# Kernel optimization log

Hardware: AMD Instinct MI355X
Metric: run time of the kernel (lower is better)

The kernel has to match this reference:

```python
import jax, jax.numpy as jnp
import numpy as np

D, N, F_IN, F_OUT = 2, 4096, 128, 128
DENSITY = 0.005  # avg degree ~20 per row in the 0/1 attention graphs
NEG_INF = -1e30


def setup_inputs() -> dict:
    key = jax.random.key(0)
    ks = jax.random.split(key, 12)
    X = jax.random.normal(ks[0], (D, N, F_IN), dtype=jnp.float32)
    # Dense Laplacian operator used in torch.sparse.mm(L[i], h_p); scaled so tanh stays non-degenerate
    L = jax.random.normal(ks[1], (D, N, N), dtype=jnp.float32) / np.float32(np.sqrt(N))
    # Upper/lower adjacency: 0/1 matrices (GATLayer extracts edges via adj == 1)
    L_u = (jax.random.uniform(ks[2], (D, N, N)) < DENSITY).astype(jnp.float32)
    L_d = (jax.random.uniform(ks[3], (D, N, N)) < DENSITY).astype(jnp.float32)
    s = np.float32(0.05)
    Wp = jax.random.normal(ks[4], (D, F_IN, F_OUT), dtype=jnp.float32) * s
    Ws = jax.random.normal(ks[5], (D, F_IN, F_OUT), dtype=jnp.float32) * s
    Wu = jax.random.normal(ks[6], (D, F_IN, F_OUT), dtype=jnp.float32) * s
    au1 = jax.random.normal(ks[7], (D, F_OUT), dtype=jnp.float32) * s
    au2 = jax.random.normal(ks[8], (D, F_OUT), dtype=jnp.float32) * s
    Wd = jax.random.normal(ks[9], (D, F_IN, F_OUT), dtype=jnp.float32) * s
    ad1 = jax.random.normal(ks[10], (D, F_OUT), dtype=jnp.float32) * s
    ad2 = jax.random.normal(ks[11], (D, F_OUT), dtype=jnp.float32) * s
    return {"X": X, "L": L, "L_u": L_u, "L_d": L_d,
            "Wp": Wp, "Ws": Ws, "Wu": Wu, "au1": au1, "au2": au2,
            "Wd": Wd, "ad1": ad1, "ad2": ad2, "dimensions": D}


def _gat(x, adj, W, a1, a2):
    # GATLayer.forward with boundary=False: linear -> edge scores -> LeakyReLU ->
    # row-wise softmax restricted to adj==1 entries -> sparse mm.
    h = x @ W                                   # [N, F_OUT]
    s1 = h @ a1                                 # [N]  (a_1 linear, bias=False)
    s2 = h @ a2                                 # [N]
    scores = jax.nn.leaky_relu(s1[:, None] + s2[None, :])  # [N, N], slope 0.01
    mask = adj == 1.0
    scores = jnp.where(mask, scores, NEG_INF)
    attn = jax.nn.softmax(scores, axis=1)
    attn = jnp.where(mask, attn, 0.0)           # zero rows with no edges (sparse softmax semantics)
    return attn @ h                             # [N, F_OUT]


def _san_dim(x, L, Lu, Ld, Wp, Ws, Wu, au1, au2, Wd, ad1, ad2):
    h_p = jnp.tanh(L @ (x @ Wp))
    h_s = jnp.tanh(x @ Ws)
    h_u = jnp.tanh(_gat(x, Lu, Wu, au1, au2))
    h_d = jnp.tanh(_gat(x, Ld, Wd, ad1, ad2))
    return h_s + h_u + h_d + h_p


def reference(X, L, L_u, L_d, Wp, Ws, Wu, au1, au2, Wd, ad1, ad2, dimensions):
    # vmap over the `dimensions` simplex levels (all per-level params stacked on axis 0)
    return jax.vmap(_san_dim)(X, L, L_u, L_d, Wp, Ws, Wu, au1, au2, Wd, ad1, ad2)
```

## Files before the change

### kernel.cpp

```cpp
#include <hip/hip_runtime.h>
#include <hip/hip_bf16.h>

#define NN 4096
#define FD 128
#define NDIM 2
#define CAP 256

#define OFF_HMAT 0
#define OFF_SVEC 3145728
#define OFF_HP   3178496
#define OFF_GU   7372800
#define OFF_GD   8421376
#define OFF_H0T  9469952

typedef _Float16 f16x8 __attribute__((ext_vector_type(8)));
typedef float f32x4 __attribute__((ext_vector_type(4)));

union P4 { _Float16 h[4]; int2 i2; };

__device__ __forceinline__ float f4get(const float4& v, int j) {
    return j == 0 ? v.x : j == 1 ? v.y : j == 2 ? v.z : v.w;
}

__global__ __launch_bounds__(256) void k_xw(
    const float* __restrict__ X, const float* __restrict__ Wp,
    const float* __restrict__ Wsm, const float* __restrict__ Wu,
    const float* __restrict__ Wd, float* __restrict__ hmat,
    _Float16* __restrict__ h0T) {
  int d = blockIdx.z, p = blockIdx.y;
  int r0 = blockIdx.x * 128;
  const float* W = (p == 0 ? Wp : p == 1 ? Wsm : p == 2 ? Wu : Wd) + (size_t)d * FD * FD;
  const float* Xd = X + ((size_t)d * NN + r0) * FD;
  __shared__ int4 As4[2048];
  __shared__ int4 Bs4[2048];
  char* As = (char*)As4; char* Bs = (char*)Bs4;
  int t = threadIdx.x;

#pragma unroll 4
  for (int u = 0; u < 16; u++) {
    int id = t + u * 256;
    int row = id >> 5, k4 = (id & 31) * 4;
    float4 v = *(const float4*)(Xd + (size_t)row * FD + k4);
    P4 pk;
    pk.h[0] = (_Float16)v.x; pk.h[1] = (_Float16)v.y;
    pk.h[2] = (_Float16)v.z; pk.h[3] = (_Float16)v.w;
    int off = (row * 256 + k4 * 2) ^ ((row & 7) << 4);
    *(int2*)(As + off) = pk.i2;
  }
#pragma unroll 4
  for (int u = 0; u < 16; u++) {
    int id = t + u * 256;
    int k = id >> 5, n4 = (id & 31) * 4;
    float4 v = *(const float4*)(W + (size_t)k * FD + n4);
#pragma unroll
    for (int j = 0; j < 4; j++) {
      int n = n4 + j;
      int off = (n * 256 + k * 2) ^ ((n & 7) << 4);
      *(_Float16*)(Bs + off) = (_Float16)f4get(v, j);
    }
  }
  __syncthreads();

  int w = t >> 6, l = t & 63;
  int lr = l & 15, lkb = (l >> 4) * 16;
  f32x4 acc[2][8] = {};
#pragma unroll
  for (int kb = 0; kb < 4; kb++) {
    f16x8 a[2], b[8];
#pragma unroll
    for (int m = 0; m < 2; m++) {
      int row = w * 32 + m * 16 + lr;
      int off = (row * 256 + kb * 64 + lkb) ^ ((row & 7) << 4);
      a[m] = *(const f16x8*)(As + off);
    }
#pragma unroll
    for (int n = 0; n < 8; n++) {
      int rn = n * 16 + lr;
      int off = (rn * 256 + kb * 64 + lkb) ^ ((rn & 7) << 4);
      b[n] = *(const f16x8*)(Bs + off);
    }
#pragma unroll
    for (int m = 0; m < 2; m++)
#pragma unroll
      for (int n = 0; n < 8; n++)
        acc[m][n] = __builtin_amdgcn_mfma_f32_16x16x32_f16(a[m], b[n], acc[m][n], 0, 0, 0);
  }

  if (p == 0) {
    _Float16* hT = h0T + (size_t)d * FD * NN;
#pragma unroll
    for (int m = 0; m < 2; m++)
#pragma unroll
      for (int n = 0; n < 8; n++) {
        int col = n * 16 + lr;
        int grow = r0 + w * 32 + m * 16 + (l >> 4) * 4;
        P4 pk;
#pragma unroll
        for (int r = 0; r < 4; r++) pk.h[r] = (_Float16)acc[m][n][r];
        *(int2*)(hT + (size_t)col * NN + grow) = pk.i2;
      }
  } else {
    float* o = hmat + ((size_t)(d * 3 + p - 1) * NN + r0) * FD;
#pragma unroll
    for (int m = 0; m < 2; m++)
#pragma unroll
      for (int n = 0; n < 8; n++)
#pragma unroll
        for (int r = 0; r < 4; r++)
          o[(size_t)(w * 32 + m * 16 + (l >> 4) * 4 + r) * FD + n * 16 + lr] = acc[m][n][r];
  }
}

__global__ __launch_bounds__(256) void k_svec(
    const float* __restrict__ hmat, const float* __restrict__ au1,
    const float* __restrict__ au2, const float* __restrict__ ad1,
    const float* __restrict__ ad2, float* __restrict__ svec) {
  int v = blockIdx.y, d = blockIdx.z;
  int w = threadIdx.x >> 6, lane = threadIdx.x & 63;
  int i = blockIdx.x * 4 + w;
  const float* a = (v == 0 ? au1 : v == 1 ? au2 : v == 2 ? ad1 : ad2) + (size_t)d * FD;
  const float* h = hmat + ((size_t)(d * 3 + 1 + (v >> 1)) * NN + i) * FD;
  float x = h[lane] * a[lane] + h[64 + lane] * a[64 + lane];
#pragma unroll
  for (int o = 1; o < 64; o <<= 1) x += __shfl_xor(x, o);
  if (lane == 0) svec[(size_t)(d * 4 + v) * NN + i] = x;
}

__global__ __launch_bounds__(256) void k_lgemm(
    const float* __restrict__ L, const _Float16* __restrict__ h0T,
    float* __restrict__ hp) {
  int d = blockIdx.z, ks = blockIdx.y;
  int r0 = blockIdx.x * 64;
  const float* Lr = L + (size_t)d * NN * NN;
  const _Float16* hT = h0T + (size_t)d * FD * NN;
  __shared__ int4 As4[512];
  __shared__ int4 Bs4[1024];
  char* As = (char*)As4; char* Bs = (char*)Bs4;
  int t = threadIdx.x;
  int w = t >> 6, l = t & 63;
  int lr = l & 15, lkb = (l >> 4) * 16;
  f32x4 acc[8] = {};
  int kbeg = ks * 1024;
  for (int kk = kbeg; kk < kbeg + 1024; kk += 64) {
#pragma unroll
    for (int u = 0; u < 4; u++) {
      int id = t + u * 256;
      int row = id >> 4, k4 = (id & 15) * 4;
      float4 v = *(const float4*)(Lr + (size_t)(r0 + row) * NN + kk + k4);
      P4 pk;
      pk.h[0] = (_Float16)v.x; pk.h[1] = (_Float16)v.y;
      pk.h[2] = (_Float16)v.z; pk.h[3] = (_Float16)v.w;
      int off = (row * 128 + k4 * 2) ^ ((row & 7) << 4);
      *(int2*)(As + off) = pk.i2;
    }
#pragma unroll
    for (int u = 0; u < 4; u++) {
      int id = t + u * 256;
      int n = id >> 3, k8 = (id & 7) * 8;
      int4 v = *(const int4*)(hT + (size_t)n * NN + kk + k8);
      int off = (n * 128 + k8 * 2) ^ ((n & 7) << 4);
      *(int4*)(Bs + off) = v;
    }
    __syncthreads();
#pragma unroll
    for (int kb = 0; kb < 2; kb++) {
      int row = w * 16 + lr;
      int offA = (row * 128 + kb * 64 + lkb) ^ ((row & 7) << 4);
      f16x8 a = *(const f16x8*)(As + offA);
      f16x8 b[8];
#pragma unroll
      for (int n = 0; n < 8; n++) {
        int rn = n * 16 + lr;
        int off = (rn * 128 + kb * 64 + lkb) ^ ((rn & 7) << 4);
        b[n] = *(const f16x8*)(Bs + off);
      }
#pragma unroll
      for (int n = 0; n < 8; n++)
        acc[n] = __builtin_amdgcn_mfma_f32_16x16x32_f16(a, b[n], acc[n], 0, 0, 0);
    }
    __syncthreads();
  }
  float* o = hp + ((size_t)(d * 4 + ks) * NN + r0) * FD;
#pragma unroll
  for (int n = 0; n < 8; n++)
#pragma unroll
    for (int r = 0; r < 4; r++)
      o[(size_t)(w * 16 + (l >> 4) * 4 + r) * FD + n * 16 + lr] = acc[n][r];
}

#define BAL(val, idxexpr)                                          \
  {                                                                \
    unsigned long long m = __ballot((val) == 1.0f);                \
    if (m) {                                                       \
      if ((val) == 1.0f) {                                         \
        int pos = c + __popcll(m & ((1ull << lane) - 1ull));       \
        if (pos < 64) ejt[w][pos] = (idxexpr);                     \
      }                                                            \
      c += __popcll(m);                                            \
    }                                                              \
  }

__global__ __launch_bounds__(256) void k_gat(
    const float* __restrict__ Lu, const float* __restrict__ Ldn,
    const float* __restrict__ hmat, const float* __restrict__ svec,
    float* __restrict__ gu, float* __restrict__ gd) {
  int i = blockIdx.x;
  int a = blockIdx.y, d = blockIdx.z;
  const float* Arow = (a ? Ldn : Lu) + ((size_t)d * NN + i) * (size_t)NN;
  const float* h = hmat + (size_t)(d * 3 + 1 + a) * NN * FD;
  const float* s1 = svec + (size_t)(d * 4 + 2 * a) * NN;
  const float* s2 = svec + (size_t)(d * 4 + 2 * a + 1) * NN;
  float* g = (a ? gd : gu) + ((size_t)d * NN + i) * FD;

  __shared__ int ejt[4][64];
  __shared__ int wcnt[4];
  __shared__ int ejs[CAP];
  __shared__ float wts[CAP];
  __shared__ float red[256];
  __shared__ float invs;

  int t = threadIdx.x, w = t >> 6, lane = t & 63;

  int bi = t * 16;
  float4 v0 = *(const float4*)(Arow + bi);
  float4 v1 = *(const float4*)(Arow + bi + 4);
  float4 v2 = *(const float4*)(Arow + bi + 8);
  float4 v3 = *(const float4*)(Arow + bi + 12);
  int c = 0;
  BAL(v0.x, bi + 0)  BAL(v0.y, bi + 1)  BAL(v0.z, bi + 2)  BAL(v0.w, bi + 3)
  BAL(v1.x, bi + 4)  BAL(v1.y, bi + 5)  BAL(v1.z, bi + 6)  BAL(v1.w, bi + 7)
  BAL(v2.x, bi + 8)  BAL(v2.y, bi + 9)  BAL(v2.z, bi + 10) BAL(v2.w, bi + 11)
  BAL(v3.x, bi + 12) BAL(v3.y, bi + 13) BAL(v3.z, bi + 14) BAL(v3.w, bi + 15)
  if (lane == 0) wcnt[w] = min(c, 64);
  __syncthreads();

  int c0 = wcnt[0], c1 = wcnt[1], c2 = wcnt[2], c3 = wcnt[3];
  int base = (w > 0 ? c0 : 0) + (w > 1 ? c1 : 0) + (w > 2 ? c2 : 0);
  int cnt = c0 + c1 + c2 + c3;
  int myc = wcnt[w];
  if (lane < myc) ejs[base + lane] = ejt[w][lane];
  __syncthreads();

  if (w == 0) {
    float s1i = s1[i];
    float sc0 = -1e30f, sc1 = -1e30f, sc2 = -1e30f, sc3 = -1e30f;
    if (lane < cnt)       { float x = s1i + s2[ejs[lane]];       sc0 = x > 0.f ? x : 0.01f * x; }
    if (64 + lane < cnt)  { float x = s1i + s2[ejs[64 + lane]];  sc1 = x > 0.f ? x : 0.01f * x; }
    if (128 + lane < cnt) { float x = s1i + s2[ejs[128 + lane]]; sc2 = x > 0.f ? x : 0.01f * x; }
    if (192 + lane < cnt) { float x = s1i + s2[ejs[192 + lane]]; sc3 = x > 0.f ? x : 0.01f * x; }
    float mx = fmaxf(fmaxf(sc0, sc1), fmaxf(sc2, sc3));
#pragma unroll
    for (int o = 1; o < 64; o <<= 1) mx = fmaxf(mx, __shfl_xor(mx, o));
    float p0 = 0.f, p1 = 0.f, p2 = 0.f, p3 = 0.f;
    if (lane < cnt)       { p0 = expf(sc0 - mx); wts[lane] = p0; }
    if (64 + lane < cnt)  { p1 = expf(sc1 - mx); wts[64 + lane] = p1; }
    if (128 + lane < cnt) { p2 = expf(sc2 - mx); wts[128 + lane] = p2; }
    if (192 + lane < cnt) { p3 = expf(sc3 - mx); wts[192 + lane] = p3; }
    float sum = p0 + p1 + p2 + p3;
#pragma unroll
    for (int o = 1; o < 64; o <<= 1) sum += __shfl_xor(sum, o);
    if (lane == 0) invs = (cnt > 0) ? 1.0f / sum : 0.0f;
  }
  __syncthreads();

  int col = t & 127;
  float acc = 0.0f;
  int e = t >> 7;
  for (; e + 6 < cnt; e += 8) {
    int j0 = ejs[e], j1 = ejs[e + 2], j2 = ejs[e + 4], j3 = ejs[e + 6];
    float w0 = wts[e], w1 = wts[e + 2], w2 = wts[e + 4], w3 = wts[e + 6];
    float h0 = h[(size_t)j0 * FD + col];
    float h1 = h[(size_t)j1 * FD + col];
    float h2 = h[(size_t)j2 * FD + col];
    float h3 = h[(size_t)j3 * FD + col];
    acc += w0 * h0 + w1 * h1 + w2 * h2 + w3 * h3;
  }
  for (; e < cnt; e += 2) acc += wts[e] * h[(size_t)ejs[e] * FD + col];
  red[t] = acc * invs;
  __syncthreads();
  if (t < 128) g[t] = red[t] + red[t + 128];
}

__global__ __launch_bounds__(256) void k_combine(
    const float* __restrict__ hmat, const float* __restrict__ hp,
    const float* __restrict__ gu, const float* __restrict__ gd,
    float* __restrict__ out) {
  const size_t tot4 = (size_t)NDIM * NN * FD / 4;
  for (size_t i4 = (size_t)blockIdx.x * blockDim.x + threadIdx.x; i4 < tot4;
       i4 += (size_t)gridDim.x * blockDim.x) {
    size_t i = i4 * 4;
    int d = (int)(i >> 19);
    size_t rem = i & 524287;
    float4 hs = *(const float4*)(hmat + ((size_t)(d * 3) << 19) + rem);
    float4 p0 = *(const float4*)(hp + ((size_t)(d * 4 + 0) << 19) + rem);
    float4 p1 = *(const float4*)(hp + ((size_t)(d * 4 + 1) << 19) + rem);
    float4 p2 = *(const float4*)(hp + ((size_t)(d * 4 + 2) << 19) + rem);
    float4 p3 = *(const float4*)(hp + ((size_t)(d * 4 + 3) << 19) + rem);
    float4 u = *(const float4*)(gu + ((size_t)d << 19) + rem);
    float4 dd = *(const float4*)(gd + ((size_t)d << 19) + rem);
    float4 o;
    o.x = tanhf(hs.x) + tanhf(u.x) + tanhf(dd.x) + tanhf(p0.x + p1.x + p2.x + p3.x);
    o.y = tanhf(hs.y) + tanhf(u.y) + tanhf(dd.y) + tanhf(p0.y + p1.y + p2.y + p3.y);
    o.z = tanhf(hs.z) + tanhf(u.z) + tanhf(dd.z) + tanhf(p0.z + p1.z + p2.z + p3.z);
    o.w = tanhf(hs.w) + tanhf(u.w) + tanhf(dd.w) + tanhf(p0.w + p1.w + p2.w + p3.w);
    *(float4*)(out + i) = o;
  }
}

extern "C" void kernel_launch(void* const* d_in, const int* in_sizes, int n_in,
                              void* d_out, int out_size, void* d_ws, size_t ws_size,
                              hipStream_t stream) {
  const float* X   = (const float*)d_in[0];
  const float* L   = (const float*)d_in[1];
  const float* Lu  = (const float*)d_in[2];
  const float* Ldn = (const float*)d_in[3];
  const float* Wp  = (const float*)d_in[4];
  const float* Wsm = (const float*)d_in[5];
  const float* Wu  = (const float*)d_in[6];
  const float* au1 = (const float*)d_in[7];
  const float* au2 = (const float*)d_in[8];
  const float* Wd  = (const float*)d_in[9];
  const float* ad1 = (const float*)d_in[10];
  const float* ad2 = (const float*)d_in[11];
  float* out = (float*)d_out;
  float* ws = (float*)d_ws;

  float* hmat = ws + OFF_HMAT;
  float* svec = ws + OFF_SVEC;
  float* hp   = ws + OFF_HP;
  float* gu   = ws + OFF_GU;
  float* gd   = ws + OFF_GD;
  _Float16* h0T = (_Float16*)(ws + OFF_H0T);

  k_xw<<<dim3(NN / 128, 4, NDIM), 256, 0, stream>>>(X, Wp, Wsm, Wu, Wd, hmat, h0T);
  k_svec<<<dim3(NN / 4, 4, NDIM), 256, 0, stream>>>(hmat, au1, au2, ad1, ad2, svec);
  k_lgemm<<<dim3(NN / 64, 4, NDIM), 256, 0, stream>>>(L, h0T, hp);
  k_gat<<<dim3(NN, 2, NDIM), 256, 0, stream>>>(Lu, Ldn, hmat, svec, gu, gd);
  k_combine<<<1024, 256, 0, stream>>>(hmat, hp, gu, gd, out);
}
```

Measured before the change: 130.8 us.

## Merge L-GEMM and GAT kernels into one launch with block-range dispatch

Fuses the dense L-GEMM kernel and the GAT aggregation kernel into a single grid. The first 512 blocks run the GEMM and the rest run the per-row GAT, with shared memory overlaid through a union. Both stages are memory-bound and independent, so they can now run concurrently, and one launch and the tail between them go away. The GAT softmax is also spread across all four waves with cross-wave reductions instead of running on wave 0 only, at the cost of two extra block barriers.

```diff
diff --git a/kernel.cpp b/kernel.cpp
--- a/kernel.cpp
+++ b/kernel.cpp
@@ -126,67 +126,13 @@
   if (lane == 0) svec[(size_t)(d * 4 + v) * NN + i] = x;
 }
 
-__global__ __launch_bounds__(256) void k_lgemm(
-    const float* __restrict__ L, const _Float16* __restrict__ h0T,
-    float* __restrict__ hp) {
-  int d = blockIdx.z, ks = blockIdx.y;
-  int r0 = blockIdx.x * 64;
-  const float* Lr = L + (size_t)d * NN * NN;
-  const _Float16* hT = h0T + (size_t)d * FD * NN;
-  __shared__ int4 As4[512];
-  __shared__ int4 Bs4[1024];
-  char* As = (char*)As4; char* Bs = (char*)Bs4;
-  int t = threadIdx.x;
-  int w = t >> 6, l = t & 63;
-  int lr = l & 15, lkb = (l >> 4) * 16;
-  f32x4 acc[8] = {};
-  int kbeg = ks * 1024;
-  for (int kk = kbeg; kk < kbeg + 1024; kk += 64) {
-#pragma unroll
-    for (int u = 0; u < 4; u++) {
-      int id = t + u * 256;
-      int row = id >> 4, k4 = (id & 15) * 4;
-      float4 v = *(const float4*)(Lr + (size_t)(r0 + row) * NN + kk + k4);
-      P4 pk;
-      pk.h[0] = (_Float16)v.x; pk.h[1] = (_Float16)v.y;
-      pk.h[2] = (_Float16)v.z; pk.h[3] = (_Float16)v.w;
-      int off = (row * 128 + k4 * 2) ^ ((row & 7) << 4);
-      *(int2*)(As + off) = pk.i2;
-    }
-#pragma unroll
-    for (int u = 0; u < 4; u++) {
-      int id = t + u * 256;
-      int n = id >> 3, k8 = (id & 7) * 8;
-      int4 v = *(const int4*)(hT + (size_t)n * NN + kk + k8);
-      int off = (n * 128 + k8 * 2) ^ ((n & 7) << 4);
-      *(int4*)(Bs + off) = v;
-    }
-    __syncthreads();
-#pragma unroll
-    for (int kb = 0; kb < 2; kb++) {
-      int row = w * 16 + lr;
-      int offA = (row * 128 + kb * 64 + lkb) ^ ((row & 7) << 4);
-      f16x8 a = *(const f16x8*)(As + offA);
-      f16x8 b[8];
-#pragma unroll
-      for (int n = 0; n < 8; n++) {
-        int rn = n * 16 + lr;
-        int off = (rn * 128 + kb * 64 + lkb) ^ ((rn & 7) << 4);
-        b[n] = *(const f16x8*)(Bs + off);
-      }
-#pragma unroll
-      for (int n = 0; n < 8; n++)
-        acc[n] = __builtin_amdgcn_mfma_f32_16x16x32_f16(a, b[n], acc[n], 0, 0, 0);
-    }
-    __syncthreads();
-  }
-  float* o = hp + ((size_t)(d * 4 + ks) * NN + r0) * FD;
-#pragma unroll
-  for (int n = 0; n < 8; n++)
-#pragma unroll
-    for (int r = 0; r < 4; r++)
-      o[(size_t)(w * 16 + (l >> 4) * 4 + r) * FD + n * 16 + lr] = acc[n][r];
-}
+struct GeSm { int4 As4[512]; int4 Bs4[1024]; };
+struct GatSm {
+  int ejt[4][64]; int wcnt[4];
+  int ejs[CAP]; float wts[CAP]; float red[256];
+  float wred[4]; float wred2[4];
+};
+union SMem { GeSm ge; GatSm ga; };
 
 #define BAL(val, idxexpr)                                          \
   {                                                                \
@@ -194,32 +140,87 @@
     if (m) {                                                       \
       if ((val) == 1.0f) {                                         \
         int pos = c + __popcll(m & ((1ull << lane) - 1ull));       \
-        if (pos < 64) ejt[w][pos] = (idxexpr);                     \
+        if (pos < 64) sm.ga.ejt[w][pos] = (idxexpr);               \
       }                                                            \
       c += __popcll(m);                                            \
     }                                                              \
   }
 
-__global__ __launch_bounds__(256) void k_gat(
+__global__ __launch_bounds__(256) void k_mg(
+    const float* __restrict__ L, const _Float16* __restrict__ h0T,
+    float* __restrict__ hp,
     const float* __restrict__ Lu, const float* __restrict__ Ldn,
     const float* __restrict__ hmat, const float* __restrict__ svec,
     float* __restrict__ gu, float* __restrict__ gd) {
-  int i = blockIdx.x;
-  int a = blockIdx.y, d = blockIdx.z;
+  __shared__ SMem sm;
+  int t = threadIdx.x;
+  int w = t >> 6, lane = t & 63;
+
+  if (blockIdx.x < 512) {
+    int b = blockIdx.x;
+    int r0 = (b & 63) * 64, ks = (b >> 6) & 3, d = b >> 8;
+    const float* Lr = L + (size_t)d * NN * NN;
+    const _Float16* hT = h0T + (size_t)d * FD * NN;
+    char* As = (char*)sm.ge.As4; char* Bs = (char*)sm.ge.Bs4;
+    int lr = lane & 15, lkb = (lane >> 4) * 16;
+    f32x4 acc[8] = {};
+    int kbeg = ks * 1024;
+    for (int kk = kbeg; kk < kbeg + 1024; kk += 64) {
+#pragma unroll
+      for (int u = 0; u < 4; u++) {
+        int id = t + u * 256;
+        int row = id >> 4, k4 = (id & 15) * 4;
+        float4 v = *(const float4*)(Lr + (size_t)(r0 + row) * NN + kk + k4);
+        P4 pk;
+        pk.h[0] = (_Float16)v.x; pk.h[1] = (_Float16)v.y;
+        pk.h[2] = (_Float16)v.z; pk.h[3] = (_Float16)v.w;
+        int off = (row * 128 + k4 * 2) ^ ((row & 7) << 4);
+        *(int2*)(As + off) = pk.i2;
+      }
+#pragma unroll
+      for (int u = 0; u < 4; u++) {
+        int id = t + u * 256;
+        int n = id >> 3, k8 = (id & 7) * 8;
+        int4 v = *(const int4*)(hT + (size_t)n * NN + kk + k8);
+        int off = (n * 128 + k8 * 2) ^ ((n & 7) << 4);
+        *(int4*)(Bs + off) = v;
+      }
+      __syncthreads();
+#pragma unroll
+      for (int kb = 0; kb < 2; kb++) {
+        int row = w * 16 + lr;
+        int offA = (row * 128 + kb * 64 + lkb) ^ ((row & 7) << 4);
+        f16x8 a = *(const f16x8*)(As + offA);
+        f16x8 bb[8];
+#pragma unroll
+        for (int n = 0; n < 8; n++) {
+          int rn = n * 16 + lr;
+          int off = (rn * 128 + kb * 64 + lkb) ^ ((rn & 7) << 4);
+          bb[n] = *(const f16x8*)(Bs + off);
+        }
+#pragma unroll
+        for (int n = 0; n < 8; n++)
+          acc[n] = __builtin_amdgcn_mfma_f32_16x16x32_f16(a, bb[n], acc[n], 0, 0, 0);
+      }
+      __syncthreads();
+    }
+    float* o = hp + ((size_t)(d * 4 + ks) * NN + r0) * FD;
+#pragma unroll
+    for (int n = 0; n < 8; n++)
+#pragma unroll
+      for (int r = 0; r < 4; r++)
+        o[(size_t)(w * 16 + (lane >> 4) * 4 + r) * FD + n * 16 + lr] = acc[n][r];
+    return;
+  }
+
+  int idx = blockIdx.x - 512;
+  int i = idx & (NN - 1);
+  int a = (idx >> 12) & 1, d = idx >> 13;
   const float* Arow = (a ? Ldn : Lu) + ((size_t)d * NN + i) * (size_t)NN;
   const float* h = hmat + (size_t)(d * 3 + 1 + a) * NN * FD;
   const float* s1 = svec + (size_t)(d * 4 + 2 * a) * NN;
   const float* s2 = svec + (size_t)(d * 4 + 2 * a + 1) * NN;
   float* g = (a ? gd : gu) + ((size_t)d * NN + i) * FD;
-
-  __shared__ int ejt[4][64];
-  __shared__ int wcnt[4];
-  __shared__ int ejs[CAP];
-  __shared__ float wts[CAP];
-  __shared__ float red[256];
-  __shared__ float invs;
-
-  int t = threadIdx.x, w = t >> 6, lane = t & 63;
 
   int bi = t * 16;
   float4 v0 = *(const float4*)(Arow + bi);
@@ -231,54 +232,56 @@
   BAL(v1.x, bi + 4)  BAL(v1.y, bi + 5)  BAL(v1.z, bi + 6)  BAL(v1.w, bi + 7)
   BAL(v2.x, bi + 8)  BAL(v2.y, bi + 9)  BAL(v2.z, bi + 10) BAL(v2.w, bi + 11)
   BAL(v3.x, bi + 12) BAL(v3.y, bi + 13) BAL(v3.z, bi + 14) BAL(v3.w, bi + 15)
-  if (lane == 0) wcnt[w] = min(c, 64);
-  __syncthreads();
-
-  int c0 = wcnt[0], c1 = wcnt[1], c2 = wcnt[2], c3 = wcnt[3];
+  if (lane == 0) sm.ga.wcnt[w] = min(c, 64);
+  __syncthreads();
+
+  int c0 = sm.ga.wcnt[0], c1 = sm.ga.wcnt[1], c2 = sm.ga.wcnt[2], c3 = sm.ga.wcnt[3];
   int base = (w > 0 ? c0 : 0) + (w > 1 ? c1 : 0) + (w > 2 ? c2 : 0);
   int cnt = c0 + c1 + c2 + c3;
-  int myc = wcnt[w];
-  if (lane < myc) ejs[base + lane] = ejt[w][lane];
-  __syncthreads();
-
-  if (w == 0) {
-    float s1i = s1[i];
-    float sc0 = -1e30f, sc1 = -1e30f, sc2 = -1e30f, sc3 = -1e30f;
-    if (lane < cnt)       { float x = s1i + s2[ejs[lane]];       sc0 = x > 0.f ? x : 0.01f * x; }
-    if (64 + lane < cnt)  { float x = s1i + s2[ejs[64 + lane]];  sc1 = x > 0.f ? x : 0.01f * x; }
-    if (128 + lane < cnt) { float x = s1i + s2[ejs[128 + lane]]; sc2 = x > 0.f ? x : 0.01f * x; }
-    if (192 + lane < cnt) { float x = s1i + s2[ejs[192 + lane]]; sc3 = x > 0.f ? x : 0.01f * x; }
-    float mx = fmaxf(fmaxf(sc0, sc1), fmaxf(sc2, sc3));
-#pragma unroll
-    for (int o = 1; o < 64; o <<= 1) mx = fmaxf(mx, __shfl_xor(mx, o));
-    float p0 = 0.f, p1 = 0.f, p2 = 0.f, p3 = 0.f;
-    if (lane < cnt)       { p0 = expf(sc0 - mx); wts[lane] = p0; }
-    if (64 + lane < cnt)  { p1 = expf(sc1 - mx); wts[64 + lane] = p1; }
-    if (128 + lane < cnt) { p2 = expf(sc2 - mx); wts[128 + lane] = p2; }
-    if (192 + lane < cnt) { p3 = expf(sc3 - mx); wts[192 + lane] = p3; }
-    float sum = p0 + p1 + p2 + p3;
-#pragma unroll
-    for (int o = 1; o < 64; o <<= 1) sum += __shfl_xor(sum, o);
-    if (lane == 0) invs = (cnt > 0) ? 1.0f / sum : 0.0f;
-  }
-  __syncthreads();
+  if (lane < sm.ga.wcnt[w]) sm.ga.ejs[base + lane] = sm.ga.ejt[w][lane];
+  __syncthreads();
+
+  float s1i = s1[i];
+  float sc = -1e30f;
+  if (t < cnt) {
+    float x = s1i + s2[sm.ga.ejs[t]];
+    sc = x > 0.0f ? x : 0.01f * x;
+  }
+  float mx = sc;
+#pragma unroll
+  for (int o = 1; o < 64; o <<= 1) mx = fmaxf(mx, __shfl_xor(mx, o));
+  if (lane == 0) sm.ga.wred[w] = mx;
+  __syncthreads();
+  mx = fmaxf(fmaxf(sm.ga.wred[0], sm.ga.wred[1]), fmaxf(sm.ga.wred[2], sm.ga.wred[3]));
+  float p = 0.0f;
+  if (t < cnt) {
+    p = expf(sc - mx);
+    sm.ga.wts[t] = p;
+  }
+  float sum = p;
+#pragma unroll
+  for (int o = 1; o < 64; o <<= 1) sum += __shfl_xor(sum, o);
+  if (lane == 0) sm.ga.wred2[w] = sum;
+  __syncthreads();
+  float tot = sm.ga.wred2[0] + sm.ga.wred2[1] + sm.ga.wred2[2] + sm.ga.wred2[3];
+  float inv = (cnt > 0) ? 1.0f / tot : 0.0f;
 
   int col = t & 127;
   float acc = 0.0f;
   int e = t >> 7;
   for (; e + 6 < cnt; e += 8) {
-    int j0 = ejs[e], j1 = ejs[e + 2], j2 = ejs[e + 4], j3 = ejs[e + 6];
-    float w0 = wts[e], w1 = wts[e + 2], w2 = wts[e + 4], w3 = wts[e + 6];
+    int j0 = sm.ga.ejs[e], j1 = sm.ga.ejs[e + 2], j2 = sm.ga.ejs[e + 4], j3 = sm.ga.ejs[e + 6];
+    float w0 = sm.ga.wts[e], w1 = sm.ga.wts[e + 2], w2 = sm.ga.wts[e + 4], w3 = sm.ga.wts[e + 6];
     float h0 = h[(size_t)j0 * FD + col];
     float h1 = h[(size_t)j1 * FD + col];
     float h2 = h[(size_t)j2 * FD + col];
     float h3 = h[(size_t)j3 * FD + col];
     acc += w0 * h0 + w1 * h1 + w2 * h2 + w3 * h3;
   }
-  for (; e < cnt; e += 2) acc += wts[e] * h[(size_t)ejs[e] * FD + col];
-  red[t] = acc * invs;
-  __syncthreads();
-  if (t < 128) g[t] = red[t] + red[t + 128];
+  for (; e < cnt; e += 2) acc += sm.ga.wts[e] * h[(size_t)sm.ga.ejs[e] * FD + col];
+  sm.ga.red[t] = acc * inv;
+  __syncthreads();
+  if (t < 128) g[t] = sm.ga.red[t] + sm.ga.red[t + 128];
 }
 
 __global__ __launch_bounds__(256) void k_combine(
@@ -334,7 +337,7 @@
 
   k_xw<<<dim3(NN / 128, 4, NDIM), 256, 0, stream>>>(X, Wp, Wsm, Wu, Wd, hmat, h0T);
   k_svec<<<dim3(NN / 4, 4, NDIM), 256, 0, stream>>>(hmat, au1, au2, ad1, ad2, svec);
-  k_lgemm<<<dim3(NN / 64, 4, NDIM), 256, 0, stream>>>(L, h0T, hp);
-  k_gat<<<dim3(NN, 2, NDIM), 256, 0, stream>>>(Lu, Ldn, hmat, svec, gu, gd);
+  k_mg<<<dim3(512 + NN * 2 * NDIM, 1, 1), 256, 0, stream>>>(
+      L, h0T, hp, Lu, Ldn, hmat, svec, gu, gd);
   k_combine<<<1024, 256, 0, stream>>>(hmat, hp, gu, gd, out);
 }
```

Result: slower. 165.0 us (+26.2%).
